# Optimization experiments

Hardware: AMD Instinct MI355X
Metric: run time of the kernel (lower is better)

Reference implementation:

```python
import jax, jax.numpy as jnp
import numpy as np

N_DRUG = 572
D = 512
K = 64          # neighbor_sample_size
T = 30000       # tail entities
R = 200         # relations
MAX_DEG = 32    # padded invariant_adj neighbor count
EPS = 1e-5


def setup_inputs() -> dict:
    key = jax.random.key(0)
    ks = jax.random.split(key, 10)
    return {
        "drug_embed_W": jax.random.normal(ks[0], (N_DRUG, D), jnp.float32),
        "rela_embed_W": jax.random.normal(ks[1], (R, D), jnp.float32),
        "ent_embed_W": jax.random.normal(ks[2], (T, D), jnp.float32),
        "Wa": jax.random.normal(ks[3], (D, D), jnp.float32) / np.float32(np.sqrt(D)),
        "lin_W": jax.random.normal(ks[4], (2 * D, D), jnp.float32) / np.float32(np.sqrt(2 * D)),
        "lin_b": jnp.zeros((D,), jnp.float32),
        "gamma": jnp.ones((D,), jnp.float32),
        "beta": jnp.zeros((D,), jnp.float32),
        "drug_name": jnp.arange(N_DRUG, dtype=jnp.int64 if jax.config.jax_enable_x64 else jnp.int32),
        "adj_tail": jax.random.randint(ks[5], (N_DRUG, K), 0, T),
        "adj_relation": jax.random.randint(ks[6], (N_DRUG, K), 0, R),
        "nbr_idx": jax.random.randint(ks[7], (N_DRUG, MAX_DEG), 0, N_DRUG),
        "nbr_deg": jax.random.randint(ks[8], (N_DRUG,), 0, MAX_DEG),
        "epoch": 2,
    }


def _forward(drug_embed_W, rela_embed_W, ent_embed_W, Wa, lin_W, lin_b, gamma, beta,
             drug_name, adj_tail, adj_relation, nbr_idx, nbr_deg, epoch):
    drug_e = drug_embed_W[drug_name]          # [N, D]
    rela = rela_embed_W[adj_relation]         # [N, K, D]
    ent = ent_embed_W[adj_tail]               # [N, K, D]

    # relation-aware attention over sampled neighbors (AttentionLayer)
    q = drug_e @ Wa                           # [N, D]
    scores = jnp.einsum('nd,nkd->nk', q, rela) * (1.0 / np.float32(np.sqrt(D)))
    attn = jax.nn.softmax(scores, axis=1)     # [N, K]
    agg = jnp.einsum('nk,nkd->nd', attn, ent) # [N, D]

    # Linear1: Linear(2D->D) + ReLU + BatchNorm1d (training-mode batch stats)
    h = jnp.concatenate([agg, drug_e], axis=1) @ lin_W + lin_b
    h = jax.nn.relu(h)
    mean = jnp.mean(h, axis=0)
    var = jnp.var(h, axis=0)                  # biased, as torch BN normalization
    drug_f = (h - mean) * jax.lax.rsqrt(var + EPS) * gamma + beta

    if epoch > 1:
        # sequential per-node neighbor-mean smoothing (in-place semantics)
        mask = (jnp.arange(MAX_DEG)[None, :] < nbr_deg[:, None])  # [N, MAX_DEG]

        def step(f, i):
            pos = nbr_idx[i]
            m = mask[i][:, None].astype(f.dtype)
            s = jnp.sum(f[pos] * m, axis=0)
            deg = nbr_deg[i]
            avg = s / jnp.maximum(deg, 1).astype(f.dtype)
            new = jnp.where(deg > 0, (avg + f[i]) * 0.5, f[i])
            return f.at[i].set(new), None

        drug_f, _ = jax.lax.scan(step, drug_f, jnp.arange(N_DRUG))
    return drug_f


def reference(drug_embed_W, rela_embed_W, ent_embed_W, Wa, lin_W, lin_b, gamma, beta,
              drug_name, adj_tail, adj_relation, nbr_idx, nbr_deg, epoch):
    return _forward(drug_embed_W, rela_embed_W, ent_embed_W, Wa, lin_W, lin_b, gamma, beta,
                    drug_name, adj_tail, adj_relation, nbr_idx, nbr_deg, epoch)
```

## Files before the change

### kernel.cpp

```cpp
#include <hip/hip_runtime.h>

#define N_DRUG 572
#define DIM 512
#define MAXDEG 32
#define FS 17

__global__ __launch_bounds__(256) void prep_kernel(
    const float* __restrict__ Wa, const float* __restrict__ relaW,
    const float* __restrict__ linW, float* __restrict__ linP,
    float* __restrict__ relaP)
{
    const int b = blockIdx.x;
    const int t = threadIdx.x;
    if (b < 512) {
        const int g = b * 256 + t;
        const int c = g & 511, k4 = g >> 9;
        const float4 v = make_float4(linW[(size_t)(k4 * 4 + 0) * 512 + c],
                                     linW[(size_t)(k4 * 4 + 1) * 512 + c],
                                     linW[(size_t)(k4 * 4 + 2) * 512 + c],
                                     linW[(size_t)(k4 * 4 + 3) * 512 + c]);
        *(float4*)&linP[((size_t)(c >> 6) * 256 + k4) * 256 + (c & 63) * 4] = v;
        return;
    }
    const int bb = b - 512;
    const int rb = bb >> 5, kb = bb & 31;
    const int wv = t >> 6, l = t & 63;
    const int r0 = rb * 16 + wv * 4;
    const int k0 = kb * 16;

    float a[4][8];
    #pragma unroll
    for (int rr = 0; rr < 4; ++rr) {
        const float4* ap = (const float4*)(relaW + (size_t)min(r0 + rr, 199) * 512 + l * 8);
        const float4 x = ap[0], y = ap[1];
        a[rr][0] = x.x; a[rr][1] = x.y; a[rr][2] = x.z; a[rr][3] = x.w;
        a[rr][4] = y.x; a[rr][5] = y.y; a[rr][6] = y.z; a[rr][7] = y.w;
    }
    float acc[64];
    #pragma unroll
    for (int i = 0; i < 64; ++i) acc[i] = 0.f;
    #pragma unroll
    for (int kk = 0; kk < 16; ++kk) {
        const float4* bp = (const float4*)(Wa + (size_t)(k0 + kk) * 512 + l * 8);
        const float4 x = bp[0], y = bp[1];
        const float bv[8] = {x.x, x.y, x.z, x.w, y.x, y.y, y.z, y.w};
        #pragma unroll
        for (int rr = 0; rr < 4; ++rr) {
            float s = acc[rr * 16 + kk];
            #pragma unroll
            for (int j = 0; j < 8; ++j) s = fmaf(a[rr][j], bv[j], s);
            acc[rr * 16 + kk] = s;
        }
    }
    #pragma unroll
    for (int off = 1; off <= 32; off <<= 1) {
        #pragma unroll
        for (int i = 0; i < 64; ++i) acc[i] += __shfl_xor(acc[i], off, 64);
    }
    float outv = acc[0];
    #pragma unroll
    for (int i = 1; i < 64; ++i) outv = (l == i) ? acc[i] : outv;
    const int rr = l >> 4, kk = l & 15;
    if (r0 + rr < 200) relaP[(size_t)(r0 + rr) * 512 + k0 + kk] = outv;
}

__global__ __launch_bounds__(256) void attn_kernel(
    const float* __restrict__ drugW, const float* __restrict__ relaP,
    const float* __restrict__ entW, const int* __restrict__ dn,
    const int* __restrict__ adj_tail, const int* __restrict__ adj_rel,
    float* __restrict__ cat)
{
    __shared__ float at[64];
    __shared__ int tails[64];
    __shared__ int rels[64];
    const int d = blockIdx.x;
    const int t = threadIdx.x;
    const int w = t >> 6, lane = t & 63;

    if (t < 64) {
        tails[t] = adj_tail[d * 64 + t];
        rels[t]  = adj_rel[d * 64 + t];
    }
    const int rd = dn[d];
    float qv[8];
    {
        const float4* qp = (const float4*)(drugW + (size_t)rd * 512 + lane * 8);
        const float4 x = qp[0], y = qp[1];
        qv[0] = x.x; qv[1] = x.y; qv[2] = x.z; qv[3] = x.w;
        qv[4] = y.x; qv[5] = y.y; qv[6] = y.z; qv[7] = y.w;
    }
    __syncthreads();

    #pragma unroll 4
    for (int kk = 0; kk < 16; ++kk) {
        const int k = w * 16 + kk;
        const float4* p = (const float4*)(relaP + (size_t)rels[k] * 512 + lane * 8);
        const float4 x = p[0], y = p[1];
        float s = 0.f;
        s = fmaf(qv[0], x.x, s); s = fmaf(qv[1], x.y, s);
        s = fmaf(qv[2], x.z, s); s = fmaf(qv[3], x.w, s);
        s = fmaf(qv[4], y.x, s); s = fmaf(qv[5], y.y, s);
        s = fmaf(qv[6], y.z, s); s = fmaf(qv[7], y.w, s);
        #pragma unroll
        for (int off = 32; off >= 1; off >>= 1) s += __shfl_xor(s, off, 64);
        if (lane == 0) at[k] = s * 0.0441941738241592f;
    }
    __syncthreads();

    if (w == 0) {
        const float s = at[lane];
        float m = s;
        #pragma unroll
        for (int off = 32; off >= 1; off >>= 1) m = fmaxf(m, __shfl_xor(m, off, 64));
        const float e = __expf(s - m);
        float sum = e;
        #pragma unroll
        for (int off = 32; off >= 1; off >>= 1) sum += __shfl_xor(sum, off, 64);
        at[lane] = e / sum;
    }
    __syncthreads();

    {
        const int c2 = t * 2;
        float a0 = 0.f, a1 = 0.f;
        #pragma unroll 8
        for (int k = 0; k < 64; ++k) {
            const float ak = at[k];
            const float2 e = *(const float2*)(entW + (size_t)tails[k] * 512 + c2);
            a0 = fmaf(ak, e.x, a0);
            a1 = fmaf(ak, e.y, a1);
        }
        float* o = cat + (size_t)d * 1024;
        *(float2*)&o[c2] = make_float2(a0, a1);
        const float2 de = *(const float2*)(drugW + (size_t)rd * 512 + c2);
        *(float2*)&o[512 + c2] = de;
    }
}

__global__ __launch_bounds__(512) void gemm_h(
    const float* __restrict__ A, const float* __restrict__ linP,
    const float* __restrict__ bias, float* __restrict__ out)
{
    __shared__ float red[8][8][128];
    const int t = threadIdx.x;
    const int wv = t >> 6, lane = t & 63;
    const int r0 = blockIdx.x * 8;
    const int half = lane >> 5;
    const int cw = (lane * 2) & 63;

    const float* wp = linP + ((size_t)(blockIdx.y * 2 + half) * 256 + wv * 32) * 256
                    + cw * 4;
    const float* ap[8];
    #pragma unroll
    for (int r = 0; r < 8; ++r)
        ap[r] = A + (size_t)min(r0 + r, N_DRUG - 1) * 1024 + wv * 128;

    float acc0[8] = {0.f, 0.f, 0.f, 0.f, 0.f, 0.f, 0.f, 0.f};
    float acc1[8] = {0.f, 0.f, 0.f, 0.f, 0.f, 0.f, 0.f, 0.f};
    #pragma unroll 2
    for (int k4 = 0; k4 < 32; ++k4) {
        const float4 w0 = *(const float4*)(wp + (size_t)k4 * 256);
        const float4 w1 = *(const float4*)(wp + (size_t)k4 * 256 + 4);
        #pragma unroll
        for (int r = 0; r < 8; ++r) {
            const float4 a = *(const float4*)(ap[r] + k4 * 4);
            acc0[r] = fmaf(a.x, w0.x, acc0[r]);
            acc0[r] = fmaf(a.y, w0.y, acc0[r]);
            acc0[r] = fmaf(a.z, w0.z, acc0[r]);
            acc0[r] = fmaf(a.w, w0.w, acc0[r]);
            acc1[r] = fmaf(a.x, w1.x, acc1[r]);
            acc1[r] = fmaf(a.y, w1.y, acc1[r]);
            acc1[r] = fmaf(a.z, w1.z, acc1[r]);
            acc1[r] = fmaf(a.w, w1.w, acc1[r]);
        }
    }
    #pragma unroll
    for (int r = 0; r < 8; ++r)
        *(float2*)&red[wv][r][lane * 2] = make_float2(acc0[r], acc1[r]);
    __syncthreads();

    #pragma unroll
    for (int u = 0; u < 2; ++u) {
        const int o = u * 512 + t;
        const int r = o >> 7, cc = o & 127;
        if (r0 + r < N_DRUG) {
            float v = red[0][r][cc];
            #pragma unroll
            for (int w = 1; w < 8; ++w) v += red[w][r][cc];
            v += bias[blockIdx.y * 128 + cc];
            out[(size_t)(r0 + r) * 512 + blockIdx.y * 128 + cc] = fmaxf(v, 0.f);
        }
    }
}

__global__ __launch_bounds__(512) void scan_kernel(
    float* hout, const float* __restrict__ gamma, const float* __restrict__ beta,
    const int* __restrict__ nbr_idx, const int* __restrict__ nbr_deg,
    const int* __restrict__ epoch)
{
    __shared__ float fs[(N_DRUG + 1) * FS];
    __shared__ alignas(16) unsigned short offs[N_DRUG * MAXDEG];
    __shared__ float2 ivw[N_DRUG];
    __shared__ int   mxs[N_DRUG];
    __shared__ float part[2][32][16];
    __shared__ float bnp[2][16];
    __shared__ int   genext[2];
    __shared__ int   ge0s;

    const int t  = threadIdx.x;
    const int c  = t & 15;
    const int h  = (t >> 4) & 1;
    const int j  = t >> 5;
    const int rr = t >> 4;
    const int c0 = blockIdx.x * 16;

    for (int i = t; i < N_DRUG; i += 512) {
        const int d = nbr_deg[i];
        ivw[i] = (d > 0) ? make_float2(0.5f / (float)d, 0.5f) : make_float2(0.f, 1.f);
        const int4* np = (const int4*)&nbr_idx[i * MAXDEG];
        unsigned* op = (unsigned*)&offs[i * MAXDEG];
        int mx = -1;
        #pragma unroll
        for (int u = 0; u < 8; ++u) {
            int4 qq = np[u];
            const int b = u * 4;
            qq.x = (b + 0 < d) ? qq.x : N_DRUG;
            qq.y = (b + 1 < d) ? qq.y : N_DRUG;
            qq.z = (b + 2 < d) ? qq.z : N_DRUG;
            qq.w = (b + 3 < d) ? qq.w : N_DRUG;
            mx = max(mx, (qq.x < i) ? qq.x : -1);
            mx = max(mx, (qq.y < i) ? qq.y : -1);
            mx = max(mx, (qq.z < i) ? qq.z : -1);
            mx = max(mx, (qq.w < i) ? qq.w : -1);
            op[2 * u]     = (unsigned)(qq.x * FS) | ((unsigned)(qq.y * FS) << 16);
            op[2 * u + 1] = (unsigned)(qq.z * FS) | ((unsigned)(qq.w * FS) << 16);
        }
        mxs[i] = mx;
    }

    {
        float sl = 0.f, ql = 0.f;
        for (int r = rr; r < N_DRUG; r += 32) {
            const float v = hout[(size_t)r * DIM + c0 + c];
            fs[r * FS + c] = v;
            sl += v;
            ql = fmaf(v, v, ql);
        }
        part[0][rr][c] = sl;
        part[1][rr][c] = ql;
    }
    if (t < FS) fs[N_DRUG * FS + t] = 0.f;
    __syncthreads();

    if (t < 16) {
        float s = 0.f, sq = 0.f;
        #pragma unroll
        for (int k = 0; k < 32; ++k) { s += part[0][k][t]; sq += part[1][k][t]; }
        const float mean = s * (1.f / N_DRUG);
        const float var = sq * (1.f / N_DRUG) - mean * mean;
        const float rstd = rsqrtf(var + 1e-5f);
        const float scl = gamma[c0 + t] * rstd;
        bnp[0][t] = scl;
        bnp[1][t] = beta[c0 + t] - mean * scl;
    }
    if ((t >> 6) == 7) {
        const int l = t & 63;
        const int jj = 1 + l;
        const bool flag = (l >= 15) || (jj >= N_DRUG) || (mxs[min(jj, N_DRUG - 1)] >= 0);
        const unsigned long long b = __ballot(flag) & 0xFFFFULL;
        if (l == 0) ge0s = 1 + (int)__builtin_ctzll(b);
    }
    __syncthreads();

    {
        const float scl = bnp[0][c];
        const float shf = bnp[1][c];
        for (int r = rr; r < N_DRUG; r += 32)
            fs[r * FS + c] = fmaf(fs[r * FS + c], scl, shf);
    }
    __syncthreads();

    if (epoch[0] > 1) {
        int gs = 0, ge = ge0s;
        uint4 ca, cb;
        {
            const uint4* p = (const uint4*)&offs[min(j, N_DRUG - 1) * MAXDEG + h * 16];
            ca = p[0]; cb = p[1];
        }
        int par = 0;
        while (gs < N_DRUG) {
            const bool pred = (gs + j) < ge;
            float s0 = 0.f, s1 = 0.f;
#define G2(W) { s0 += fs[(W & 0xffffu) + c]; s1 += fs[(W >> 16) + c]; }
            if (pred) { G2(ca.x) G2(ca.y) G2(ca.z) G2(ca.w)
                        G2(cb.x) G2(cb.y) G2(cb.z) G2(cb.w) }
#undef G2
            uint4 na, nb;
            {
                const uint4* p = (const uint4*)&offs[min(ge + j, N_DRUG - 1) * MAXDEG + h * 16];
                na = p[0]; nb = p[1];
            }
            float nv = 0.f;
            if (pred) {
                const float cur = fs[(gs + j) * FS + c];
                const float2 iw = ivw[gs + j];
                float sh = s0 + s1;
                sh += __shfl_xor(sh, 16, 64);
                nv = fmaf(sh, iw.x, cur * iw.y);
            }
            if ((t >> 6) == 7) {
                const int l = t & 63;
                const int jj = ge + 1 + l;
                const bool flag = (l >= 15) || (jj >= N_DRUG) ||
                                  (mxs[min(jj, N_DRUG - 1)] >= ge);
                const unsigned long long b = __ballot(flag) & 0xFFFFULL;
                if (l == 0) genext[par] = ge + 1 + (int)__builtin_ctzll(b);
            }
            __syncthreads();
            if (pred && h == 0) fs[(gs + j) * FS + c] = nv;
            __syncthreads();
            gs = ge;
            ge = genext[par];
            par ^= 1;
            ca = na; cb = nb;
        }
    }
    __syncthreads();

    for (int r = rr; r < N_DRUG; r += 32)
        hout[(size_t)r * DIM + c0 + c] = fs[r * FS + c];
}

extern "C" void kernel_launch(void* const* d_in, const int* in_sizes, int n_in,
                              void* d_out, int out_size, void* d_ws, size_t ws_size,
                              hipStream_t stream)
{
    const float* drugW = (const float*)d_in[0];
    const float* relaW = (const float*)d_in[1];
    const float* entW  = (const float*)d_in[2];
    const float* Wa    = (const float*)d_in[3];
    const float* linW  = (const float*)d_in[4];
    const float* linb  = (const float*)d_in[5];
    const float* gamma = (const float*)d_in[6];
    const float* beta  = (const float*)d_in[7];
    const int* drug_name = (const int*)d_in[8];
    const int* adj_tail  = (const int*)d_in[9];
    const int* adj_rel   = (const int*)d_in[10];
    const int* nbr_idx   = (const int*)d_in[11];
    const int* nbr_deg   = (const int*)d_in[12];
    const int* epoch     = (const int*)d_in[13];

    float* out = (float*)d_out;

    float* linP  = (float*)d_ws;
    float* relaP = (float*)((char*)d_ws + 2097152);
    float* cat   = (float*)((char*)d_ws + 2506752);

    prep_kernel<<<928, 256, 0, stream>>>(Wa, relaW, linW, linP, relaP);
    attn_kernel<<<N_DRUG, 256, 0, stream>>>(drugW, relaP, entW, drug_name,
                                            adj_tail, adj_rel, cat);
    gemm_h<<<dim3(72, 4), 512, 0, stream>>>(cat, linP, linb, out);
    scan_kernel<<<32, 512, 0, stream>>>(out, gamma, beta, nbr_idx, nbr_deg, epoch);
}
```

Before: 227.1 us.

## Make scan smoothing wave-independent per column to drop block barriers

The sequential neighbor-smoothing loop used to split rows across all waves and needed two block-wide __syncthreads per group step. It now gives each wavefront two of the 16 columns. Every wave computes its own next group boundary with a ballot and reads and writes LDS without block barriers, relying on in-wave ordering plus compiler memory fences. This is meant to remove barrier latency from the serial critical path, at the cost of redundant boundary computation in every wave and lower parallelism per row.

```diff
diff --git a/kernel.cpp b/kernel.cpp
--- a/kernel.cpp
+++ b/kernel.cpp
@@ -204,13 +204,9 @@
     __shared__ int   mxs[N_DRUG];
     __shared__ float part[2][32][16];
     __shared__ float bnp[2][16];
-    __shared__ int   genext[2];
-    __shared__ int   ge0s;
 
     const int t  = threadIdx.x;
     const int c  = t & 15;
-    const int h  = (t >> 4) & 1;
-    const int j  = t >> 5;
     const int rr = t >> 4;
     const int c0 = blockIdx.x * 16;
 
@@ -263,13 +259,6 @@
         bnp[0][t] = scl;
         bnp[1][t] = beta[c0 + t] - mean * scl;
     }
-    if ((t >> 6) == 7) {
-        const int l = t & 63;
-        const int jj = 1 + l;
-        const bool flag = (l >= 15) || (jj >= N_DRUG) || (mxs[min(jj, N_DRUG - 1)] >= 0);
-        const unsigned long long b = __ballot(flag) & 0xFFFFULL;
-        if (l == 0) ge0s = 1 + (int)__builtin_ctzll(b);
-    }
     __syncthreads();
 
     {
@@ -281,47 +270,57 @@
     __syncthreads();
 
     if (epoch[0] > 1) {
-        int gs = 0, ge = ge0s;
+        const int wv   = t >> 6;
+        const int lane = t & 63;
+        const int j    = lane >> 2;
+        const int hh   = (lane >> 1) & 1;
+        const int cl   = (wv << 1) | (lane & 1);
+
+        int gs = 0;
+        int ge;
+        {
+            const int jj = 1 + lane;
+            const bool flag = (lane >= 15) || (jj >= N_DRUG) ||
+                              (mxs[min(jj, N_DRUG - 1)] >= 0);
+            ge = 1 + (int)__builtin_ctzll(__ballot(flag) & 0xFFFFULL);
+        }
         uint4 ca, cb;
         {
-            const uint4* p = (const uint4*)&offs[min(j, N_DRUG - 1) * MAXDEG + h * 16];
+            const uint4* p = (const uint4*)&offs[j * MAXDEG + hh * 16];
             ca = p[0]; cb = p[1];
         }
-        int par = 0;
         while (gs < N_DRUG) {
             const bool pred = (gs + j) < ge;
             float s0 = 0.f, s1 = 0.f;
-#define G2(W) { s0 += fs[(W & 0xffffu) + c]; s1 += fs[(W >> 16) + c]; }
+#define G2(W) { s0 += fs[(W & 0xffffu) + cl]; s1 += fs[(W >> 16) + cl]; }
             if (pred) { G2(ca.x) G2(ca.y) G2(ca.z) G2(ca.w)
                         G2(cb.x) G2(cb.y) G2(cb.z) G2(cb.w) }
 #undef G2
             uint4 na, nb;
             {
-                const uint4* p = (const uint4*)&offs[min(ge + j, N_DRUG - 1) * MAXDEG + h * 16];
+                const uint4* p = (const uint4*)&offs[min(ge + j, N_DRUG - 1) * MAXDEG + hh * 16];
                 na = p[0]; nb = p[1];
+            }
+            int genext;
+            {
+                const int jj = ge + 1 + lane;
+                const bool flag = (lane >= 15) || (jj >= N_DRUG) ||
+                                  (mxs[min(jj, N_DRUG - 1)] >= ge);
+                genext = ge + 1 + (int)__builtin_ctzll(__ballot(flag) & 0xFFFFULL);
             }
             float nv = 0.f;
             if (pred) {
-                const float cur = fs[(gs + j) * FS + c];
+                const float cur = fs[(gs + j) * FS + cl];
                 const float2 iw = ivw[gs + j];
                 float sh = s0 + s1;
-                sh += __shfl_xor(sh, 16, 64);
+                sh += __shfl_xor(sh, 2, 64);
                 nv = fmaf(sh, iw.x, cur * iw.y);
             }
-            if ((t >> 6) == 7) {
-                const int l = t & 63;
-                const int jj = ge + 1 + l;
-                const bool flag = (l >= 15) || (jj >= N_DRUG) ||
-                                  (mxs[min(jj, N_DRUG - 1)] >= ge);
-                const unsigned long long b = __ballot(flag) & 0xFFFFULL;
-                if (l == 0) genext[par] = ge + 1 + (int)__builtin_ctzll(b);
-            }
-            __syncthreads();
-            if (pred && h == 0) fs[(gs + j) * FS + c] = nv;
-            __syncthreads();
+            asm volatile("" ::: "memory");
+            if (pred && hh == 0) fs[(gs + j) * FS + cl] = nv;
+            asm volatile("" ::: "memory");
             gs = ge;
-            ge = genext[par];
-            par ^= 1;
+            ge = genext;
             ca = na; cb = nb;
         }
     }
```

Measured after the change: 226.4 us. About the same (-0.3%).
